# Optimization experiments

Measured on AMD Instinct MI355X. Metric: run time of the kernel, lower is better.

## Reference

```python
import jax, jax.numpy as jnp
import numpy as np

K1, K2, K3 = 6, 4, 3  # knn_graph k (loop=True -> self included, dist 0 is always top)


def _sqdist(a, b):
    # a: [B,N,3], b: [B,M,3] -> [B,N,M] squared euclidean distances
    an = jnp.sum(a * a, -1)[:, :, None]
    bn = jnp.sum(b * b, -1)[:, None, :]
    return an + bn - 2.0 * jnp.einsum('bnd,bmd->bnm', a, b)


def _knn_idx(pos, k):
    # for each point, indices of its k nearest neighbors (self included, loop=True)
    d = _sqdist(pos, pos)                 # [B,N,N]
    _, idx = jax.lax.top_k(-d, k)         # [B,N,k]
    return idx


def _gather(a, idx):
    # a: [B,N,...], idx: [B,...] -> per-cloud gather
    return jax.vmap(lambda ab, ib: ab[ib])(a, idx)


def _fps(pos, m):
    # farthest point sampling on one cloud [N,3], deterministic start at index 0
    min_d = jnp.sum((pos - pos[0]) ** 2, -1)  # [N]

    def step(min_d, _):
        idx = jnp.argmax(min_d)
        d = jnp.sum((pos - pos[idx]) ** 2, -1)
        return jnp.minimum(min_d, d), idx

    _, idxs = jax.lax.scan(step, min_d, None, length=m - 1)
    return jnp.concatenate([jnp.zeros((1,), dtype=idxs.dtype), idxs])


def _pn_layer(h, pos, k, W1, b1, W2, b2):
    # PointNetLayer: gather h_i/h_j/pos_i/pos_j over knn edges, MLP, max-aggregate
    idx = _knn_idx(pos, k)                       # [B,N,k]
    h_j = _gather(h, idx)                        # [B,N,k,C]
    pos_j = _gather(pos, idx)                    # [B,N,k,3]
    rel = pos_j - pos[:, :, None, :]             # pos_j - pos_i
    h_i = jnp.broadcast_to(h[:, :, None, :], h_j.shape)
    inp = jnp.concatenate([h_i, h_j, rel], -1)   # [B,N,k,2C+3]
    msg = jnp.maximum(inp @ W1 + b1, 0.0) @ W2 + b2
    return jnp.max(msg, axis=2)                  # scatter-max == dense max over k


def _forward(x, pos, W11, b11, W12, b12, W21, b21, W22, b22, W31, b31, W32, b32, Wr, br):
    h = jax.nn.relu(_pn_layer(x, pos, K1, W11, b11, W12, b12))
    idx = jax.vmap(lambda p: _fps(p, p.shape[0] // 2))(pos)   # ratio=0.5
    pos, h = _gather(pos, idx), _gather(h, idx)
    h = jax.nn.relu(_pn_layer(h, pos, K2, W21, b21, W22, b22))
    idx = jax.vmap(lambda p: _fps(p, p.shape[0] // 2))(pos)
    pos, h = _gather(pos, idx), _gather(h, idx)
    h = jax.nn.relu(_pn_layer(h, pos, K3, W31, b31, W32, b32))
    g = jnp.max(h, axis=1)                        # global_max_pool
    return g @ Wr + br                            # [B,10]


def _lin(key, fin, fout):
    k1, k2 = jax.random.split(key)
    lim = 1.0 / np.sqrt(fin)
    W = jax.random.uniform(k1, (fin, fout), minval=-lim, maxval=lim, dtype=jnp.float32)
    b = jax.random.uniform(k2, (fout,), minval=-lim, maxval=lim, dtype=jnp.float32)
    return W, b


def setup_inputs() -> dict:
    key = jax.random.key(0)
    ks = jax.random.split(key, 10)
    B, N = 16, 4096
    x = jax.random.normal(ks[0], (B, N, 1), dtype=jnp.float32)
    pos = jax.random.uniform(ks[1], (B, N, 3), dtype=jnp.float32)
    W11, b11 = _lin(ks[2], 1 * 2 + 3, 32)
    W12, b12 = _lin(ks[3], 32, 32)
    W21, b21 = _lin(ks[4], 32 * 2 + 3, 32)
    W22, b22 = _lin(ks[5], 32, 32)
    W31, b31 = _lin(ks[6], 32 * 2 + 3, 32)
    W32, b32 = _lin(ks[7], 32, 32)
    Wr, br = _lin(ks[8], 32, 10)
    return dict(x=x, pos=pos, W11=W11, b11=b11, W12=W12, b12=b12,
                W21=W21, b21=b21, W22=W22, b22=b22,
                W31=W31, b31=b31, W32=W32, b32=b32, Wr=Wr, br=br)


def reference(x, pos, W11, b11, W12, b12, W21, b21, W22, b22, W31, b31, W32, b32, Wr, br):
    return _forward(x, pos, W11, b11, W12, b12, W21, b21, W22, b22,
                    W31, b31, W32, b32, Wr, br)
```

## Files before the change

kernel.cpp:

```cpp
#include <hip/hip_runtime.h>

#define BATCH 16
#define NP1 4096
#define NP2 2048
#define NP3 1024

typedef float v2f __attribute__((ext_vector_type(2)));

__device__ __forceinline__ float f_add(float a, float b) { return __fadd_rn(a, b); }
__device__ __forceinline__ float f_mul(float a, float b) { return __fmul_rn(a, b); }
__device__ __forceinline__ float f_sub(float a, float b) { return __fsub_rn(a, b); }
__device__ __forceinline__ float sqnorm3(float x, float y, float z) {
  return f_add(f_add(f_mul(x, x), f_mul(y, y)), f_mul(z, z));
}

__device__ __forceinline__ unsigned long long u64max(unsigned long long a,
                                                     unsigned long long b) {
  return a > b ? a : b;
}
__device__ __forceinline__ unsigned long long u64min(unsigned long long a,
                                                     unsigned long long b) {
  return a < b ? a : b;
}
__device__ __forceinline__ double dmax(double a, double b) { return __builtin_fmax(a, b); }

template<int CTRL, int RMASK>
__device__ __forceinline__ unsigned long long dpp_u64(unsigned long long k) {
  const int lo = __builtin_amdgcn_update_dpp(0, (int)(unsigned)k, CTRL, RMASK, 0xF, true);
  const int hi = __builtin_amdgcn_update_dpp(0, (int)(unsigned)(k >> 32), CTRL, RMASK, 0xF, true);
  return ((unsigned long long)(unsigned)hi << 32) | (unsigned)lo;
}
template<int CTRL, int RMASK>
__device__ __forceinline__ double dpp_dbl(double v) {
  return __longlong_as_double(
      (long long)dpp_u64<CTRL, RMASK>((unsigned long long)__double_as_longlong(v)));
}


__device__ __forceinline__ double wave_max_keyd(double k) {
  k = dmax(k, dpp_dbl<0x111, 0xF>(k));
  k = dmax(k, dpp_dbl<0x112, 0xF>(k));
  k = dmax(k, dpp_dbl<0x114, 0xF>(k));
  k = dmax(k, dpp_dbl<0x118, 0xF>(k));
  k = dmax(k, dpp_dbl<0x142, 0xA>(k));
  k = dmax(k, dpp_dbl<0x143, 0xC>(k));
  return k;
}

template<int N, int M>
__device__ void fps_block(char* __restrict__ smem, const float* __restrict__ P,
                          int* __restrict__ samp, float* __restrict__ pos_out)
{
#pragma clang fp contract(off)
  constexpr int THREADS = 512;
  constexpr int E = N / THREADS;
  constexpr int P2 = E / 2;
  float4* pos4 = (float4*)smem;
  unsigned short* ord = (unsigned short*)(smem + 16 * N);
  int* sampL = (int*)(smem + 18 * N);
  unsigned* cursor = (unsigned*)(smem + 18 * N + 4 * M);
  double* kslots = (double*)(smem + 18 * N + 4 * M + 32);
  const int tid = threadIdx.x;
  const int lane = tid & 63, wv = tid >> 6;
  const int myslot = lane & 7;
  if (tid < 8) cursor[tid] = 0u;
  __syncthreads();
  int oct[E];
#pragma unroll
  for (int e = 0; e < E; ++e) {
    const int t = e * THREADS + tid;
    const float x = P[t * 3], y = P[t * 3 + 1], z = P[t * 3 + 2];
    pos4[t] = make_float4(x, y, z, 0.f);
    oct[e] = (x > 0.5f ? 1 : 0) | (y > 0.5f ? 2 : 0) | (z > 0.5f ? 4 : 0);
    atomicAdd(&cursor[oct[e]], 1u);
  }
  __syncthreads();
  if (tid == 0) {
    unsigned run = 0;
#pragma unroll
    for (int o = 0; o < 8; ++o) { const unsigned c = cursor[o]; cursor[o] = run; run += c; }
  }
  __syncthreads();
#pragma unroll
  for (int e = 0; e < E; ++e) {
    const unsigned d = atomicAdd(&cursor[oct[e]], 1u);
    ord[d] = (unsigned short)(e * THREADS + tid);
  }
  __syncthreads();
  const float4 p0 = pos4[0];
  const float x0 = p0.x, y0 = p0.y, z0 = p0.z;
  v2f X2[P2], Y2[P2], Z2[P2], MD2[P2];
  unsigned ILO[E];
  double key;
  float mnx = 1e30f, mny = 1e30f, mnz = 1e30f;
  float mxx = -1e30f, mxy = -1e30f, mxz = -1e30f;
  {
    double ka = 0.0, kb = 0.0;
    const v2f x0v = {x0, x0}, y0v = {y0, y0}, z0v = {z0, z0};
#pragma unroll
    for (int p = 0; p < P2; ++p) {
      const int q0 = wv * (64 * E) + (2 * p) * 64 + lane;
      const int o0 = ord[q0], o1 = ord[q0 + 64];
      const float4 a0 = pos4[o0], a1 = pos4[o1];
      X2[p] = (v2f){a0.x, a1.x}; Y2[p] = (v2f){a0.y, a1.y}; Z2[p] = (v2f){a0.z, a1.z};
      mnx = fminf(mnx, fminf(a0.x, a1.x)); mxx = fmaxf(mxx, fmaxf(a0.x, a1.x));
      mny = fminf(mny, fminf(a0.y, a1.y)); mxy = fmaxf(mxy, fmaxf(a0.y, a1.y));
      mnz = fminf(mnz, fminf(a0.z, a1.z)); mxz = fmaxf(mxz, fmaxf(a0.z, a1.z));
      const v2f dx = X2[p] - x0v, dy = Y2[p] - y0v, dz = Z2[p] - z0v;
      MD2[p] = (dx * dx + dy * dy) + dz * dz;
      ILO[2 * p]     = 0xFFFFFFFFu - (unsigned)o0;
      ILO[2 * p + 1] = 0xFFFFFFFFu - (unsigned)o1;
      const unsigned long long k0 =
          ((unsigned long long)__float_as_uint(MD2[p].x) << 32) | ILO[2 * p];
      const unsigned long long k1 =
          ((unsigned long long)__float_as_uint(MD2[p].y) << 32) | ILO[2 * p + 1];
      const double kp = dmax(__longlong_as_double((long long)k0),
                             __longlong_as_double((long long)k1));
      if (p & 1) kb = dmax(kb, kp); else ka = dmax(ka, kp);
    }
    key = dmax(ka, kb);
  }
#pragma unroll
  for (int off = 1; off < 64; off <<= 1) {
    mnx = fminf(mnx, __shfl_xor(mnx, off)); mxx = fmaxf(mxx, __shfl_xor(mxx, off));
    mny = fminf(mny, __shfl_xor(mny, off)); mxy = fmaxf(mxy, __shfl_xor(mxy, off));
    mnz = fminf(mnz, __shfl_xor(mnz, off)); mxz = fmaxf(mxz, __shfl_xor(mxz, off));
  }
  if (tid == 0) sampL[0] = 0;
  bool dirty = true;
  double wkey = 0.0;
#pragma unroll 1
  for (int s = 1; s < M; ++s) {
    if (dirty) wkey = wave_max_keyd(key);
    const int pb = s & 1;
    if (lane == 63) kslots[pb * 8 + wv] = wkey;
    __syncthreads();
    double v = kslots[pb * 8 + myslot];
    v = dmax(v, dpp_dbl<0xB1, 0xF>(v));
    v = dmax(v, dpp_dbl<0x4E, 0xF>(v));
    v = dmax(v, dpp_dbl<0x124, 0xF>(v));
    const unsigned long long kb = (unsigned long long)__double_as_longlong(v);
    const int gi = (int)(0xFFFFFFFFu - (unsigned)kb);
    const float4 sp = pos4[gi];
    if (tid == 0) sampL[s] = gi;
    const float mdx = fmaxf(fmaxf(f_sub(mnx, sp.x), f_sub(sp.x, mxx)), 0.f);
    const float mdy = fmaxf(fmaxf(f_sub(mny, sp.y), f_sub(sp.y, mxy)), 0.f);
    const float mdz = fmaxf(fmaxf(f_sub(mnz, sp.z), f_sub(sp.z, mxz)), 0.f);
    const float mind2 = sqnorm3(mdx, mdy, mdz);
    const unsigned wmhi = (unsigned)__builtin_amdgcn_readlane(
        (int)(unsigned)((unsigned long long)__double_as_longlong(wkey) >> 32), 63);
    const float wmaxf = __uint_as_float(wmhi);
    if (mind2 < wmaxf) {
      dirty = true;
      double ka = 0.0, kb2 = 0.0;
      const v2f sxv = {sp.x, sp.x}, syv = {sp.y, sp.y}, szv = {sp.z, sp.z};
#pragma unroll
      for (int p = 0; p < P2; ++p) {
        const v2f dx = X2[p] - sxv, dy = Y2[p] - syv, dz = Z2[p] - szv;
        const v2f d = (dx * dx + dy * dy) + dz * dz;
        MD2[p] = __builtin_elementwise_min(MD2[p], d);
        const unsigned long long k0 =
            ((unsigned long long)__float_as_uint(MD2[p].x) << 32) | ILO[2 * p];
        const unsigned long long k1 =
            ((unsigned long long)__float_as_uint(MD2[p].y) << 32) | ILO[2 * p + 1];
        const double kp = dmax(__longlong_as_double((long long)k0),
                               __longlong_as_double((long long)k1));
        if (p & 1) kb2 = dmax(kb2, kp); else ka = dmax(ka, kp);
      }
      key = dmax(ka, kb2);
    } else {
      dirty = false;
    }
  }
  __syncthreads();
  for (int s2 = tid; s2 < M; s2 += THREADS) {
    const int g = sampL[s2];
    samp[s2] = g;
    const float4 sp2 = pos4[g];
    pos_out[3 * s2 + 0] = sp2.x;
    pos_out[3 * s2 + 1] = sp2.y;
    pos_out[3 * s2 + 2] = sp2.z;
  }
}

__device__ __forceinline__ float f4c(const float4& v, int c) {
  return c == 0 ? v.x : c == 1 ? v.y : c == 2 ? v.z : v.w;
}
__device__ __forceinline__ void fma4(float4& a, float v, const float4& w) {
  a.x += v * w.x; a.y += v * w.y; a.z += v * w.z; a.w += v * w.w;
}

template<int K, int C>
__device__ void pn_compute(
    const float4* __restrict__ sW1, const float4* __restrict__ sW2,
    const float* __restrict__ sb1, const float* __restrict__ sb2,
    const float* __restrict__ P, const float* __restrict__ Hsrc,
    const int* __restrict__ hmap, int i, float xi, float yi, float zi,
    const int* kn, float* __restrict__ outrow)
{
  float4 abase[8];
#pragma unroll
  for (int o = 0; o < 8; ++o)
    abase[o] = make_float4(sb1[4 * o], sb1[4 * o + 1], sb1[4 * o + 2], sb1[4 * o + 3]);
  if constexpr (C == 1) {
    const float v = Hsrc[hmap ? hmap[i] : i];
#pragma unroll
    for (int o = 0; o < 8; ++o) fma4(abase[o], v, sW1[o]);
  } else {
    const int ri = hmap ? hmap[i] : i;
    const float4* Hi = (const float4*)(Hsrc + (size_t)ri * C);
#pragma unroll
    for (int c4 = 0; c4 < C / 4; ++c4) {
      const float4 hv = Hi[c4];
#pragma unroll
      for (int q = 0; q < 4; ++q) {
        const float v = f4c(hv, q);
#pragma unroll
        for (int o = 0; o < 8; ++o) fma4(abase[o], v, sW1[(4 * c4 + q) * 8 + o]);
      }
    }
  }
  float4 best[8];
#pragma unroll
  for (int o = 0; o < 8; ++o)
    best[o] = make_float4(-__builtin_inff(), -__builtin_inff(), -__builtin_inff(), -__builtin_inff());

  auto edge_pair = [&](int j0, int j1) {
    float4 a0[8], a1[8];
#pragma unroll
    for (int o = 0; o < 8; ++o) { a0[o] = abase[o]; a1[o] = abase[o]; }
    const float rx0 = P[j0 * 3] - xi, ry0 = P[j0 * 3 + 1] - yi, rz0 = P[j0 * 3 + 2] - zi;
    const float rx1 = P[j1 * 3] - xi, ry1 = P[j1 * 3 + 1] - yi, rz1 = P[j1 * 3 + 2] - zi;
    if constexpr (C == 1) {
      const float v0 = Hsrc[hmap ? hmap[j0] : j0], v1 = Hsrc[hmap ? hmap[j1] : j1];
#pragma unroll
      for (int o = 0; o < 8; ++o) {
        const float4 w = sW1[C * 8 + o];
        fma4(a0[o], v0, w); fma4(a1[o], v1, w);
      }
    } else {
      const int r0i = hmap ? hmap[j0] : j0, r1i = hmap ? hmap[j1] : j1;
      const float4* Hj0 = (const float4*)(Hsrc + (size_t)r0i * C);
      const float4* Hj1 = (const float4*)(Hsrc + (size_t)r1i * C);
#pragma unroll
      for (int c4 = 0; c4 < C / 4; ++c4) {
        const float4 h0 = Hj0[c4], h1 = Hj1[c4];
#pragma unroll
        for (int q = 0; q < 4; ++q) {
          const float v0 = f4c(h0, q), v1 = f4c(h1, q);
#pragma unroll
          for (int o = 0; o < 8; ++o) {
            const float4 w = sW1[(C + 4 * c4 + q) * 8 + o];
            fma4(a0[o], v0, w); fma4(a1[o], v1, w);
          }
        }
      }
    }
    const float r0[3] = {rx0, ry0, rz0}, r1[3] = {rx1, ry1, rz1};
#pragma unroll
    for (int r = 0; r < 3; ++r) {
#pragma unroll
      for (int o = 0; o < 8; ++o) {
        const float4 w = sW1[(2 * C + r) * 8 + o];
        fma4(a0[o], r0[r], w); fma4(a1[o], r1[r], w);
      }
    }
#pragma unroll
    for (int o = 0; o < 8; ++o) {
      a0[o].x = fmaxf(a0[o].x, 0.f); a0[o].y = fmaxf(a0[o].y, 0.f);
      a0[o].z = fmaxf(a0[o].z, 0.f); a0[o].w = fmaxf(a0[o].w, 0.f);
      a1[o].x = fmaxf(a1[o].x, 0.f); a1[o].y = fmaxf(a1[o].y, 0.f);
      a1[o].z = fmaxf(a1[o].z, 0.f); a1[o].w = fmaxf(a1[o].w, 0.f);
    }
#pragma unroll
    for (int hf = 0; hf < 2; ++hf) {
      float4 m0[4], m1[4];
#pragma unroll
      for (int o4 = 0; o4 < 4; ++o4) {
        const int c0 = 16 * hf + 4 * o4;
        m0[o4] = make_float4(sb2[c0], sb2[c0 + 1], sb2[c0 + 2], sb2[c0 + 3]);
        m1[o4] = m0[o4];
      }
#pragma unroll
      for (int c = 0; c < 32; ++c) {
        const float v0 = f4c(a0[c >> 2], c & 3), v1 = f4c(a1[c >> 2], c & 3);
#pragma unroll
        for (int o4 = 0; o4 < 4; ++o4) {
          const float4 w = sW2[c * 8 + hf * 4 + o4];
          fma4(m0[o4], v0, w); fma4(m1[o4], v1, w);
        }
      }
#pragma unroll
      for (int o4 = 0; o4 < 4; ++o4) {
        float4& bb = best[hf * 4 + o4];
        bb.x = fmaxf(bb.x, fmaxf(m0[o4].x, m1[o4].x));
        bb.y = fmaxf(bb.y, fmaxf(m0[o4].y, m1[o4].y));
        bb.z = fmaxf(bb.z, fmaxf(m0[o4].z, m1[o4].z));
        bb.w = fmaxf(bb.w, fmaxf(m0[o4].w, m1[o4].w));
      }
    }
  };

#pragma unroll
  for (int e = 0; e + 1 < K; e += 2) edge_pair(kn[e], kn[e + 1]);

  float4* ho = (float4*)outrow;
#pragma unroll
  for (int o = 0; o < 8; ++o)
    ho[o] = make_float4(fmaxf(best[o].x, 0.0f), fmaxf(best[o].y, 0.0f),
                        fmaxf(best[o].z, 0.0f), fmaxf(best[o].w, 0.0f));
}

template<int K, int NC, int C, int THREADS>
__device__ void fused_knn_pn(char* __restrict__ smem,
    const float* __restrict__ P, const float* __restrict__ Hsrc,
    const int* __restrict__ hmap,
    const float* __restrict__ W1, const float* __restrict__ b1,
    const float* __restrict__ W2, const float* __restrict__ b2,
    float* __restrict__ hout, int s)
{
  constexpr int CIN = 2 * C + 3;
  float4* tile = (float4*)smem;
  float4* sW1 = (float4*)(smem + 16 * 1024);
  float4* sW2 = sW1 + CIN * 8;
  float* sb1 = (float*)(sW2 + 32 * 8);
  float* sb2 = sb1 + 32;
  const int tid = threadIdx.x;
  for (int t = tid; t < CIN * 8; t += THREADS) sW1[t] = ((const float4*)W1)[t];
  for (int t = tid; t < 32 * 8; t += THREADS) sW2[t] = ((const float4*)W2)[t];
  if (tid < 32) { sb1[tid] = b1[tid]; sb2[tid] = b2[tid]; }

  const float xi = P[s * 3], yi = P[s * 3 + 1], zi = P[s * 3 + 2];
  const float ni = sqnorm3(xi, yi, zi);
  float bd[K]; int bj[K];
#pragma unroll
  for (int t = 0; t < K; ++t) { bd[t] = __builtin_inff(); bj[t] = 0; }
  for (int base = 0; base < NC; base += 1024) {
    __syncthreads();
    for (int t = tid; t < 1024; t += THREADS) {
      const float* q = P + (size_t)(base + t) * 3;
      const float x = q[0], y = q[1], z = q[2];
      tile[t] = make_float4(x, y, z, sqnorm3(x, y, z));
    }
    __syncthreads();
#pragma unroll 1
    for (int t = 0; t < 1024; t += 8) {
      float dv[8];
#pragma unroll
      for (int u = 0; u < 8; ++u) {
        const float4 q = tile[t + u];
        const float dot = f_add(f_add(f_mul(xi, q.x), f_mul(yi, q.y)), f_mul(zi, q.z));
        dv[u] = f_sub(f_add(ni, q.w), f_mul(2.0f, dot));
      }
#pragma unroll
      for (int u = 0; u < 8; ++u) {
        if (dv[u] < bd[K - 1]) {
          bd[K - 1] = dv[u]; bj[K - 1] = base + t + u;
#pragma unroll
          for (int r = K - 1; r > 0; --r) {
            if (bd[r] < bd[r - 1]) {
              float td = bd[r]; bd[r] = bd[r - 1]; bd[r - 1] = td;
              int   tj = bj[r]; bj[r] = bj[r - 1]; bj[r - 1] = tj;
            } else break;
          }
        }
      }
    }
  }
  pn_compute<K, C>(sW1, sW2, sb1, sb2, P, Hsrc, hmap, s, xi, yi, zi, bj,
                   hout + (size_t)s * 32);
}

template<int K, int NC>
__device__ void fused_knn_pn_quad(char* __restrict__ smem,
    const float* __restrict__ P, const float* __restrict__ Hsrc,
    const int* __restrict__ hmap,
    const float* __restrict__ W1, const float* __restrict__ b1,
    const float* __restrict__ W2, const float* __restrict__ b2,
    float* __restrict__ hout, int s, int q)
{
  constexpr int THREADS = 256;
  constexpr int RQ = NC / 4;
  constexpr int CIN = 67;
  float4* tile = (float4*)smem;
  float4* sW1 = (float4*)(smem + 16 * (NC + 4));
  float4* sW2 = sW1 + CIN * 8;
  float* sb1 = (float*)(sW2 + 32 * 8);
  float* sb2 = sb1 + 32;
  const int tid = threadIdx.x;

  for (int t = tid; t < NC; t += THREADS) {
    const float* c = P + (size_t)t * 3;
    const float x = c[0], y = c[1], z = c[2];
    tile[t + t / RQ] = make_float4(x, y, z, sqnorm3(x, y, z));
  }
  for (int t = tid; t < CIN * 8; t += THREADS) sW1[t] = ((const float4*)W1)[t];
  for (int t = tid; t < 32 * 8; t += THREADS) sW2[t] = ((const float4*)W2)[t];
  if (tid < 32) { sb1[tid] = b1[tid]; sb2[tid] = b2[tid]; }
  __syncthreads();

  const float4 qv = tile[s + s / RQ];
  const float xi = qv.x, yi = qv.y, zi = qv.z, ni = qv.w;

  const int ri = hmap ? hmap[s] : s;
  float4 hi4[8];
  {
    const float4* Hi = (const float4*)(Hsrc + (size_t)ri * 32);
#pragma unroll
    for (int c4 = 0; c4 < 8; ++c4) hi4[c4] = Hi[c4];
  }

  float bd[4]; int bj[4];
#pragma unroll
  for (int t = 0; t < 4; ++t) { bd[t] = __builtin_inff(); bj[t] = 0; }
  const int sbase = q * (RQ + 1);
#pragma unroll 1
  for (int t = 0; t < RQ; t += 8) {
    float dv[8];
#pragma unroll
    for (int u = 0; u < 8; ++u) {
      const float4 c = tile[sbase + t + u];
      const float dot = f_add(f_add(f_mul(xi, c.x), f_mul(yi, c.y)), f_mul(zi, c.z));
      dv[u] = f_sub(f_add(ni, c.w), f_mul(2.0f, dot));
    }
#pragma unroll
    for (int u = 0; u < 8; ++u) {
      if (dv[u] < bd[3]) {
        bd[3] = dv[u]; bj[3] = q * RQ + t + u;
#pragma unroll
        for (int r = 3; r > 0; --r) {
          if (bd[r] < bd[r - 1]) {
            float td = bd[r]; bd[r] = bd[r - 1]; bd[r - 1] = td;
            int   tj = bj[r]; bj[r] = bj[r - 1]; bj[r - 1] = tj;
          } else break;
        }
      }
    }
  }
  unsigned long long a0, a1, a2, a3;
  {
    auto mk = [](float d, int j) {
      unsigned u = __float_as_uint(d);
      u ^= (unsigned)((int)u >> 31) | 0x80000000u;
      return ((unsigned long long)u << 32) | (unsigned)j;
    };
    a0 = mk(bd[0], bj[0]); a1 = mk(bd[1], bj[1]);
    a2 = mk(bd[2], bj[2]); a3 = mk(bd[3], bj[3]);
  }
  {
    const unsigned long long b0 = __shfl_xor(a0, 1), b1_ = __shfl_xor(a1, 1),
                             b2_ = __shfl_xor(a2, 1), b3_ = __shfl_xor(a3, 1);
    const unsigned long long t0 = u64min(a0, b3_), t1 = u64min(a1, b2_),
                             t2 = u64min(a2, b1_), t3 = u64min(a3, b0);
    const unsigned long long u0 = u64min(t0, t2), u2 = u64max(t0, t2),
                             u1 = u64min(t1, t3), u3 = u64max(t1, t3);
    a0 = u64min(u0, u1); a1 = u64max(u0, u1);
    a2 = u64min(u2, u3); a3 = u64max(u2, u3);
  }
  {
    const unsigned long long b0 = __shfl_xor(a0, 2), b1_ = __shfl_xor(a1, 2),
                             b2_ = __shfl_xor(a2, 2), b3_ = __shfl_xor(a3, 2);
    const unsigned long long t0 = u64min(a0, b3_), t1 = u64min(a1, b2_),
                             t2 = u64min(a2, b1_), t3 = u64min(a3, b0);
    const unsigned long long u0 = u64min(t0, t2), u2 = u64max(t0, t2),
                             u1 = u64min(t1, t3), u3 = u64max(t1, t3);
    a0 = u64min(u0, u1); a1 = u64max(u0, u1);
    a2 = u64min(u2, u3); a3 = u64max(u2, u3);
  }
  const int e = (q < K) ? q : (K - 1);
  const unsigned long long ke = (e == 0) ? a0 : (e == 1) ? a1 : (e == 2) ? a2 : a3;
  const int jn = (int)(unsigned)ke;

  const int rj = hmap ? hmap[jn] : jn;
  float4 hj4[8];
  {
    const float4* Hj = (const float4*)(Hsrc + (size_t)rj * 32);
#pragma unroll
    for (int c4 = 0; c4 < 8; ++c4) hj4[c4] = Hj[c4];
  }
  float4 acc[8];
#pragma unroll
  for (int o = 0; o < 8; ++o)
    acc[o] = make_float4(sb1[4 * o], sb1[4 * o + 1], sb1[4 * o + 2], sb1[4 * o + 3]);
#pragma unroll
  for (int c4 = 0; c4 < 8; ++c4) {
    const float4 hv = hi4[c4];
#pragma unroll
    for (int t = 0; t < 4; ++t) {
      const float v = f4c(hv, t);
#pragma unroll
      for (int o = 0; o < 8; ++o) fma4(acc[o], v, sW1[(4 * c4 + t) * 8 + o]);
    }
  }
#pragma unroll
  for (int c4 = 0; c4 < 8; ++c4) {
    const float4 hv = hj4[c4];
#pragma unroll
    for (int t = 0; t < 4; ++t) {
      const float v = f4c(hv, t);
#pragma unroll
      for (int o = 0; o < 8; ++o) fma4(acc[o], v, sW1[(32 + 4 * c4 + t) * 8 + o]);
    }
  }
  const float4 cj = tile[jn + jn / RQ];
  const float r3[3] = {cj.x - xi, cj.y - yi, cj.z - zi};
#pragma unroll
  for (int r = 0; r < 3; ++r)
#pragma unroll
    for (int o = 0; o < 8; ++o) fma4(acc[o], r3[r], sW1[(64 + r) * 8 + o]);
#pragma unroll
  for (int o = 0; o < 8; ++o) {
    acc[o].x = fmaxf(acc[o].x, 0.f); acc[o].y = fmaxf(acc[o].y, 0.f);
    acc[o].z = fmaxf(acc[o].z, 0.f); acc[o].w = fmaxf(acc[o].w, 0.f);
  }
  float4 m[8];
#pragma unroll
  for (int o = 0; o < 8; ++o)
    m[o] = make_float4(sb2[4 * o], sb2[4 * o + 1], sb2[4 * o + 2], sb2[4 * o + 3]);
#pragma unroll
  for (int c = 0; c < 32; ++c) {
    const float v = f4c(acc[c >> 2], c & 3);
#pragma unroll
    for (int o = 0; o < 8; ++o) fma4(m[o], v, sW2[c * 8 + o]);
  }
#pragma unroll
  for (int o = 0; o < 8; ++o) {
    float4 v = m[o];
    v.x = fmaxf(v.x, __shfl_xor(v.x, 1)); v.y = fmaxf(v.y, __shfl_xor(v.y, 1));
    v.z = fmaxf(v.z, __shfl_xor(v.z, 1)); v.w = fmaxf(v.w, __shfl_xor(v.w, 1));
    v.x = fmaxf(v.x, __shfl_xor(v.x, 2)); v.y = fmaxf(v.y, __shfl_xor(v.y, 2));
    v.z = fmaxf(v.z, __shfl_xor(v.z, 2)); v.w = fmaxf(v.w, __shfl_xor(v.w, 2));
    m[o] = v;
  }
  float4* ho = (float4*)(hout + (size_t)s * 32);
  {
    const float4 v0 = m[2 * q], v1 = m[2 * q + 1];
    ho[2 * q] = make_float4(fmaxf(v0.x, 0.f), fmaxf(v0.y, 0.f),
                            fmaxf(v0.z, 0.f), fmaxf(v0.w, 0.f));
    ho[2 * q + 1] = make_float4(fmaxf(v1.x, 0.f), fmaxf(v1.y, 0.f),
                                fmaxf(v1.z, 0.f), fmaxf(v1.w, 0.f));
  }
}

__global__ __launch_bounds__(512) void megaA(
    const float* __restrict__ x, const float* __restrict__ pos,
    const float* __restrict__ W11, const float* __restrict__ b11,
    const float* __restrict__ W12, const float* __restrict__ b12,
    int* __restrict__ samp1, float* __restrict__ pos2, float* __restrict__ h1full)
{
  __shared__ __align__(16) char smem[82112];
  if (blockIdx.x < BATCH) {
    const int b = blockIdx.x;
    fps_block<NP1, NP2>(smem, pos + (size_t)b * NP1 * 3, samp1 + b * NP2,
                        pos2 + (size_t)b * NP2 * 3);
  } else {
    const int id = blockIdx.x - BATCH;
    const int b = id >> 3;
    const int s = (id & 7) * 512 + threadIdx.x;
    fused_knn_pn<6, NP1, 1, 512>(smem, pos + (size_t)b * NP1 * 3, x + (size_t)b * NP1,
                                 nullptr, W11, b11, W12, b12,
                                 h1full + (size_t)b * NP1 * 32, s);
  }
}

__global__ __launch_bounds__(256) void megaB(
    const float* __restrict__ pos2, const int* __restrict__ samp1,
    const float* __restrict__ h1full,
    const float* __restrict__ W21, const float* __restrict__ b21,
    const float* __restrict__ W22, const float* __restrict__ b22,
    float* __restrict__ h2out)
{
  __shared__ __align__(16) char smem[(2048 + 4) * 16 + 67 * 8 * 16 + 32 * 8 * 16 + 256];
  const int b = blockIdx.x >> 4;
  const int s = ((blockIdx.x & 15) << 6) + (threadIdx.x >> 2);
  const int q = threadIdx.x & 3;
  fused_knn_pn_quad<4, NP2>(smem, pos2 + (size_t)b * NP2 * 3,
                            h1full + (size_t)b * NP1 * 32, samp1 + b * NP2,
                            W21, b21, W22, b22, h2out + (size_t)b * NP3 * 32, s, q);
}

__global__ __launch_bounds__(256) void megaC(
    const float* __restrict__ pos2, const float* __restrict__ h2out,
    const float* __restrict__ W31, const float* __restrict__ b31,
    const float* __restrict__ W32, const float* __restrict__ b32,
    float* __restrict__ h3full)
{
  __shared__ __align__(16) char smem[(1024 + 4) * 16 + 67 * 8 * 16 + 32 * 8 * 16 + 256];
  const int b = blockIdx.x >> 4;
  const int s = ((blockIdx.x & 15) << 6) + (threadIdx.x >> 2);
  const int q = threadIdx.x & 3;
  fused_knn_pn_quad<3, NP3>(smem, pos2 + (size_t)b * NP2 * 3,
                            h2out + (size_t)b * NP3 * 32, nullptr,
                            W31, b31, W32, b32, h3full + (size_t)b * NP3 * 32, s, q);
}

__global__ __launch_bounds__(256) void final_kernel(
    const float* __restrict__ h, const float* __restrict__ Wr,
    const float* __restrict__ br, float* __restrict__ out)
{
  __shared__ float red[8][32];
  __shared__ float g[32];
  const int b = blockIdx.x;
  const int c = threadIdx.x & 31, grp = threadIdx.x >> 5;
  const float* H = h + (size_t)b * NP3 * 32;
  float m = -__builtin_inff();
  for (int r = grp; r < NP3; r += 8) m = fmaxf(m, H[r * 32 + c]);
  red[grp][c] = m;
  __syncthreads();
  if (threadIdx.x < 32) {
    float v = red[0][c];
#pragma unroll
    for (int w = 1; w < 8; ++w) v = fmaxf(v, red[w][c]);
    g[c] = v;
  }
  __syncthreads();
  if (threadIdx.x < 10) {
    float v = br[threadIdx.x];
#pragma unroll
    for (int cc = 0; cc < 32; ++cc) v += g[cc] * Wr[cc * 10 + threadIdx.x];
    out[b * 10 + threadIdx.x] = v;
  }
}

extern "C" void kernel_launch(void* const* d_in, const int* in_sizes, int n_in,
                              void* d_out, int out_size, void* d_ws, size_t ws_size,
                              hipStream_t stream) {
  const float* x   = (const float*)d_in[0];
  const float* pos = (const float*)d_in[1];
  const float* W11 = (const float*)d_in[2];
  const float* b11 = (const float*)d_in[3];
  const float* W12 = (const float*)d_in[4];
  const float* b12 = (const float*)d_in[5];
  const float* W21 = (const float*)d_in[6];
  const float* b21 = (const float*)d_in[7];
  const float* W22 = (const float*)d_in[8];
  const float* b22 = (const float*)d_in[9];
  const float* W31 = (const float*)d_in[10];
  const float* b31 = (const float*)d_in[11];
  const float* W32 = (const float*)d_in[12];
  const float* b32 = (const float*)d_in[13];
  const float* Wr  = (const float*)d_in[14];
  const float* br  = (const float*)d_in[15];
  float* out = (float*)d_out;

  char* p = (char*)d_ws;
  auto alloc = [&](size_t bytes) {
    char* r = p; p += (bytes + 255) & ~(size_t)255; return r;
  };
  int*   samp1  = (int*)  alloc(sizeof(int)   * BATCH * NP2);
  float* pos2   = (float*)alloc(sizeof(float) * BATCH * NP2 * 3);
  float* h1full = (float*)alloc(sizeof(float) * BATCH * NP1 * 32);
  float* h2out  = (float*)alloc(sizeof(float) * BATCH * NP3 * 32);
  float* h3full = (float*)alloc(sizeof(float) * BATCH * NP3 * 32);

  megaA<<<BATCH + BATCH * (NP1 / 512), 512, 0, stream>>>(
      x, pos, W11, b11, W12, b12, samp1, pos2, h1full);
  megaB<<<BATCH * 16, 256, 0, stream>>>(
      pos2, samp1, h1full, W21, b21, W22, b22, h2out);
  megaC<<<BATCH * 16, 256, 0, stream>>>(
      pos2, h2out, W31, b31, W32, b32, h3full);
  final_kernel<<<BATCH, 256, 0, stream>>>(h3full, Wr, br, out);
}
```

Before: 1.359 ms.

## Speculatively select two FPS samples per iteration using top-2 reduction

The farthest point sampling loop now reduces a top-2 key pair across the block instead of a single max. When the second candidate is at least as far from the first as its own current min-distance, both can be taken in one iteration, so that iteration needs only one block barrier. This roughly halves the serial synchronized iterations, at the cost of a heavier reduction (two doubles per DPP stage) and extra shared memory for the key slots.

```diff
diff --git a/kernel.cpp b/kernel.cpp
--- a/kernel.cpp
+++ b/kernel.cpp
@@ -23,6 +23,7 @@
   return a < b ? a : b;
 }
 __device__ __forceinline__ double dmax(double a, double b) { return __builtin_fmax(a, b); }
+__device__ __forceinline__ double dmin(double a, double b) { return __builtin_fmin(a, b); }
 
 template<int CTRL, int RMASK>
 __device__ __forceinline__ unsigned long long dpp_u64(unsigned long long k) {
@@ -37,14 +38,17 @@
 }
 
 
-__device__ __forceinline__ double wave_max_keyd(double k) {
-  k = dmax(k, dpp_dbl<0x111, 0xF>(k));
-  k = dmax(k, dpp_dbl<0x112, 0xF>(k));
-  k = dmax(k, dpp_dbl<0x114, 0xF>(k));
-  k = dmax(k, dpp_dbl<0x118, 0xF>(k));
-  k = dmax(k, dpp_dbl<0x142, 0xA>(k));
-  k = dmax(k, dpp_dbl<0x143, 0xC>(k));
-  return k;
+__device__ __forceinline__ void tup_comb(double& a1, double& a2, double b1, double b2) {
+  const double hi = dmax(a1, b1);
+  const double lo = dmin(a1, b1);
+  a2 = dmax(lo, dmax(a2, b2));
+  a1 = hi;
+}
+template<int CTRL, int RMASK>
+__device__ __forceinline__ void tup_stage(double& a1, double& a2) {
+  const double b1 = dpp_dbl<CTRL, RMASK>(a1);
+  const double b2 = dpp_dbl<CTRL, RMASK>(a2);
+  tup_comb(a1, a2, b1, b2);
 }
 
 template<int N, int M>
@@ -91,11 +95,9 @@
   const float x0 = p0.x, y0 = p0.y, z0 = p0.z;
   v2f X2[P2], Y2[P2], Z2[P2], MD2[P2];
   unsigned ILO[E];
-  double key;
   float mnx = 1e30f, mny = 1e30f, mnz = 1e30f;
   float mxx = -1e30f, mxy = -1e30f, mxz = -1e30f;
   {
-    double ka = 0.0, kb = 0.0;
     const v2f x0v = {x0, x0}, y0v = {y0, y0}, z0v = {z0, z0};
 #pragma unroll
     for (int p = 0; p < P2; ++p) {
@@ -110,15 +112,7 @@
       MD2[p] = (dx * dx + dy * dy) + dz * dz;
       ILO[2 * p]     = 0xFFFFFFFFu - (unsigned)o0;
       ILO[2 * p + 1] = 0xFFFFFFFFu - (unsigned)o1;
-      const unsigned long long k0 =
-          ((unsigned long long)__float_as_uint(MD2[p].x) << 32) | ILO[2 * p];
-      const unsigned long long k1 =
-          ((unsigned long long)__float_as_uint(MD2[p].y) << 32) | ILO[2 * p + 1];
-      const double kp = dmax(__longlong_as_double((long long)k0),
-                             __longlong_as_double((long long)k1));
-      if (p & 1) kb = dmax(kb, kp); else ka = dmax(ka, kp);
-    }
-    key = dmax(ka, kb);
+    }
   }
 #pragma unroll
   for (int off = 1; off < 64; off <<= 1) {
@@ -128,49 +122,91 @@
   }
   if (tid == 0) sampL[0] = 0;
   bool dirty = true;
-  double wkey = 0.0;
+  double W1 = 0.0, W2 = 0.0;
+  int s = 1, it = 0;
 #pragma unroll 1
-  for (int s = 1; s < M; ++s) {
-    if (dirty) wkey = wave_max_keyd(key);
-    const int pb = s & 1;
-    if (lane == 63) kslots[pb * 8 + wv] = wkey;
+  while (s < M) {
+    if (dirty) {
+      double k[E];
+#pragma unroll
+      for (int p = 0; p < P2; ++p) {
+        k[2 * p] = __longlong_as_double((long long)(
+            ((unsigned long long)__float_as_uint(MD2[p].x) << 32) | ILO[2 * p]));
+        k[2 * p + 1] = __longlong_as_double((long long)(
+            ((unsigned long long)__float_as_uint(MD2[p].y) << 32) | ILO[2 * p + 1]));
+      }
+      double A1 = dmax(k[0], k[1]), A2 = dmin(k[0], k[1]);
+      double B1 = dmax(k[2], k[3]), B2 = dmin(k[2], k[3]);
+      double C1 = dmax(k[4], k[5]), C2 = dmin(k[4], k[5]);
+      double D1 = dmax(k[6], k[7]), D2 = dmin(k[6], k[7]);
+      tup_comb(A1, A2, B1, B2); tup_comb(C1, C2, D1, D2); tup_comb(A1, A2, C1, C2);
+      tup_stage<0x111, 0xF>(A1, A2);
+      tup_stage<0x112, 0xF>(A1, A2);
+      tup_stage<0x114, 0xF>(A1, A2);
+      tup_stage<0x118, 0xF>(A1, A2);
+      tup_stage<0x142, 0xA>(A1, A2);
+      tup_stage<0x143, 0xC>(A1, A2);
+      W1 = A1; W2 = A2;
+    }
+    const int pb = it & 1;
+    if (lane == 63) ((double2*)kslots)[pb * 8 + wv] = make_double2(W1, W2);
     __syncthreads();
-    double v = kslots[pb * 8 + myslot];
-    v = dmax(v, dpp_dbl<0xB1, 0xF>(v));
-    v = dmax(v, dpp_dbl<0x4E, 0xF>(v));
-    v = dmax(v, dpp_dbl<0x124, 0xF>(v));
-    const unsigned long long kb = (unsigned long long)__double_as_longlong(v);
-    const int gi = (int)(0xFFFFFFFFu - (unsigned)kb);
-    const float4 sp = pos4[gi];
-    if (tid == 0) sampL[s] = gi;
-    const float mdx = fmaxf(fmaxf(f_sub(mnx, sp.x), f_sub(sp.x, mxx)), 0.f);
-    const float mdy = fmaxf(fmaxf(f_sub(mny, sp.y), f_sub(sp.y, mxy)), 0.f);
-    const float mdz = fmaxf(fmaxf(f_sub(mnz, sp.z), f_sub(sp.z, mxz)), 0.f);
-    const float mind2 = sqnorm3(mdx, mdy, mdz);
-    const unsigned wmhi = (unsigned)__builtin_amdgcn_readlane(
-        (int)(unsigned)((unsigned long long)__double_as_longlong(wkey) >> 32), 63);
-    const float wmaxf = __uint_as_float(wmhi);
-    if (mind2 < wmaxf) {
+    double2 tt = ((double2*)kslots)[pb * 8 + myslot];
+    double T1 = tt.x, T2 = tt.y;
+    tup_stage<0xB1, 0xF>(T1, T2);
+    tup_stage<0x4E, 0xF>(T1, T2);
+    tup_stage<0x124, 0xF>(T1, T2);
+    const unsigned long long g1b = (unsigned long long)__double_as_longlong(T1);
+    const unsigned long long g2b = (unsigned long long)__double_as_longlong(T2);
+    const int gi1 = (int)(0xFFFFFFFFu - (unsigned)g1b);
+    const int gi2 = (int)(0xFFFFFFFFu - (unsigned)g2b);
+    const float4 sp1 = pos4[gi1];
+    const float4 sp2 = pos4[gi2];
+    const float md2b = __uint_as_float((unsigned)(g2b >> 32));
+    const float ddx = f_sub(sp2.x, sp1.x), ddy = f_sub(sp2.y, sp1.y),
+                ddz = f_sub(sp2.z, sp1.z);
+    const float dchk = f_add(f_add(f_mul(ddx, ddx), f_mul(ddy, ddy)), f_mul(ddz, ddz));
+    const bool take2 = (s + 1 < M) && (dchk >= md2b);
+    if (tid == 0) { sampL[s] = gi1; if (take2) sampL[s + 1] = gi2; }
+    const float wmaxf = __uint_as_float((unsigned)__builtin_amdgcn_readlane(
+        (int)(unsigned)((unsigned long long)__double_as_longlong(W1) >> 32), 63));
+    const float m1x = fmaxf(fmaxf(f_sub(mnx, sp1.x), f_sub(sp1.x, mxx)), 0.f);
+    const float m1y = fmaxf(fmaxf(f_sub(mny, sp1.y), f_sub(sp1.y, mxy)), 0.f);
+    const float m1z = fmaxf(fmaxf(f_sub(mnz, sp1.z), f_sub(sp1.z, mxz)), 0.f);
+    const bool u1 = sqnorm3(m1x, m1y, m1z) < wmaxf;
+    const float m2x = fmaxf(fmaxf(f_sub(mnx, sp2.x), f_sub(sp2.x, mxx)), 0.f);
+    const float m2y = fmaxf(fmaxf(f_sub(mny, sp2.y), f_sub(sp2.y, mxy)), 0.f);
+    const float m2z = fmaxf(fmaxf(f_sub(mnz, sp2.z), f_sub(sp2.z, mxz)), 0.f);
+    const bool u2 = take2 && (sqnorm3(m2x, m2y, m2z) < wmaxf);
+    if (u1 | u2) {
       dirty = true;
-      double ka = 0.0, kb2 = 0.0;
-      const v2f sxv = {sp.x, sp.x}, syv = {sp.y, sp.y}, szv = {sp.z, sp.z};
-#pragma unroll
-      for (int p = 0; p < P2; ++p) {
-        const v2f dx = X2[p] - sxv, dy = Y2[p] - syv, dz = Z2[p] - szv;
-        const v2f d = (dx * dx + dy * dy) + dz * dz;
-        MD2[p] = __builtin_elementwise_min(MD2[p], d);
-        const unsigned long long k0 =
-            ((unsigned long long)__float_as_uint(MD2[p].x) << 32) | ILO[2 * p];
-        const unsigned long long k1 =
-            ((unsigned long long)__float_as_uint(MD2[p].y) << 32) | ILO[2 * p + 1];
-        const double kp = dmax(__longlong_as_double((long long)k0),
-                               __longlong_as_double((long long)k1));
-        if (p & 1) kb2 = dmax(kb2, kp); else ka = dmax(ka, kp);
-      }
-      key = dmax(ka, kb2);
+      if (u1 & u2) {
+        const v2f s1x = {sp1.x, sp1.x}, s1y = {sp1.y, sp1.y}, s1z = {sp1.z, sp1.z};
+        const v2f s2x = {sp2.x, sp2.x}, s2y = {sp2.y, sp2.y}, s2z = {sp2.z, sp2.z};
+#pragma unroll
+        for (int p = 0; p < P2; ++p) {
+          const v2f dx1 = X2[p] - s1x, dy1 = Y2[p] - s1y, dz1 = Z2[p] - s1z;
+          const v2f d1 = (dx1 * dx1 + dy1 * dy1) + dz1 * dz1;
+          MD2[p] = __builtin_elementwise_min(MD2[p], d1);
+          const v2f dx2 = X2[p] - s2x, dy2 = Y2[p] - s2y, dz2 = Z2[p] - s2z;
+          const v2f d2 = (dx2 * dx2 + dy2 * dy2) + dz2 * dz2;
+          MD2[p] = __builtin_elementwise_min(MD2[p], d2);
+        }
+      } else {
+        const float4 sp = u1 ? sp1 : sp2;
+        const v2f sxv = {sp.x, sp.x}, syv = {sp.y, sp.y}, szv = {sp.z, sp.z};
+#pragma unroll
+        for (int p = 0; p < P2; ++p) {
+          const v2f dx = X2[p] - sxv, dy = Y2[p] - syv, dz = Z2[p] - szv;
+          const v2f d = (dx * dx + dy * dy) + dz * dz;
+          MD2[p] = __builtin_elementwise_min(MD2[p], d);
+        }
+      }
     } else {
       dirty = false;
     }
+    s += take2 ? 2 : 1;
+    ++it;
   }
   __syncthreads();
   for (int s2 = tid; s2 < M; s2 += THREADS) {
@@ -548,7 +584,7 @@
     const float* __restrict__ W12, const float* __restrict__ b12,
     int* __restrict__ samp1, float* __restrict__ pos2, float* __restrict__ h1full)
 {
-  __shared__ __align__(16) char smem[82112];
+  __shared__ __align__(16) char smem[82240];
   if (blockIdx.x < BATCH) {
     const int b = blockIdx.x;
     fps_block<NP1, NP2>(smem, pos + (size_t)b * NP1 * 3, samp1 + b * NP2,
```

After: 1.325 ms. -2.5%, faster.
